# Performance work log

Measured on AMD Instinct MI355X. Metric: run time of the kernel, lower is better.

Reference implementation:

```python
import jax, jax.numpy as jnp
import numpy as np

D_MODEL = 1024
D_STATE = 16
DT_RANK = 64  # ceil(1024/16)
DT_MIN, DT_MAX = 1e-3, 1e-1


def setup_inputs() -> dict:
    key = jax.random.key(0)
    ks = jax.random.split(key, 6)
    x = jax.random.normal(ks[0], (2, 2048, D_MODEL), jnp.float32)
    A_log = jax.random.normal(ks[1], (D_MODEL, D_STATE), jnp.float32)
    D = jax.random.normal(ks[2], (D_MODEL,), jnp.float32)
    # nn.Linear default init ~ U(-1/sqrt(fan_in), 1/sqrt(fan_in)); normal*scale is fine for a baseline
    x_proj_w = jax.random.normal(ks[3], (DT_RANK + 2 * D_STATE, D_MODEL), jnp.float32) * (D_MODEL ** -0.5)
    dt_init_std = DT_RANK ** -0.5
    dt_proj_w = jax.random.uniform(ks[4], (D_MODEL, DT_RANK), jnp.float32, -dt_init_std, dt_init_std)
    dt = jnp.exp(jax.random.uniform(ks[5], (D_MODEL,), jnp.float32)
                 * (np.log(DT_MAX) - np.log(DT_MIN)) + np.log(DT_MIN))
    dt_proj_b = dt + jnp.log(-jnp.expm1(-dt))  # inverse-softplus init
    return {"x": x, "A_log": A_log, "D": D, "x_proj_w": x_proj_w,
            "dt_proj_w": dt_proj_w, "dt_proj_b": dt_proj_b}


def _s6(x, A_log, D, x_proj_w, dt_proj_w, dt_proj_b):
    A = -jnp.exp(A_log)                                    # (d, n)
    xp = jnp.einsum('bld,ed->ble', x, x_proj_w)            # (b, l, r+2n)
    d_rank = xp[..., :DT_RANK]
    Bm = xp[..., DT_RANK:DT_RANK + D_STATE]                # (b, l, n)
    Cm = xp[..., DT_RANK + D_STATE:]                       # (b, l, n)
    delta = jax.nn.softplus(jnp.einsum('blr,dr->bld', d_rank, dt_proj_w) + dt_proj_b)
    deltaA = jnp.exp(jnp.einsum('bld,dn->bldn', delta, A))          # (b, l, d, n)
    deltaB_u = jnp.einsum('bld,bln,bld->bldn', delta, Bm, x)        # (b, l, d, n)

    def step(h, inp):
        dA_t, dBu_t, C_t = inp          # (b,d,n), (b,d,n), (b,n)
        h = dA_t * h + dBu_t
        y = jnp.einsum('bdn,bn->bd', h, C_t)
        return h, y

    b, l, d = x.shape
    h0 = jnp.zeros((b, d, D_STATE), x.dtype)
    _, ys = jax.lax.scan(step, h0,
                         (deltaA.transpose(1, 0, 2, 3),
                          deltaB_u.transpose(1, 0, 2, 3),
                          Cm.transpose(1, 0, 2)))
    y = ys.transpose(1, 0, 2) + x * D                      # (b, l, d)
    return y


def reference(x, A_log, D, x_proj_w, dt_proj_w, dt_proj_b):
    return _s6(x, A_log, D, x_proj_w, dt_proj_w, dt_proj_b)
```

## Files before the change

### kernel.cpp

```cpp
#include <hip/hip_runtime.h>
#include <math.h>

#define Bb 2
#define Ll 2048
#define Dm 1024
#define Ns 16
#define Rr 64
#define Ee 96
#define XPS 8
#define BLK (Bb*Ll)
#define NTHR 256
#define LOG2E 1.4426950408889634f
#define LN2   0.6931471805599453f

__device__ inline float ex2(float x) {
#if __has_builtin(__builtin_amdgcn_exp2f)
    return __builtin_amdgcn_exp2f(x);
#else
    return exp2f(x);
#endif
}
__device__ inline float lg2(float x) {
#if __has_builtin(__builtin_amdgcn_logf)
    return __builtin_amdgcn_logf(x);
#else
    return log2f(x);
#endif
}
__device__ inline float softplus_f(float z) {
    float e = ex2(-fabsf(z) * LOG2E);
    return fmaxf(z, 0.f) + lg2(1.f + e) * LN2;
}

__global__ void __launch_bounds__(NTHR)
k_xproj(const float* __restrict__ x, const float* __restrict__ xw,
        float* __restrict__ xp_part) {
    __shared__ __align__(16) float xs[32 * 68];
    __shared__ __align__(16) float wsh[32 * 100];
    int bx = blockIdx.x;
    int ks = bx & 7, mt = bx >> 3;
    int i0 = mt * 64;
    int tid = threadIdx.x;
    int tx = tid & 15, ty = tid >> 4;
    float acc[4][6];
#pragma unroll
    for (int ii = 0; ii < 4; ++ii)
#pragma unroll
        for (int jj = 0; jj < 6; ++jj) acc[ii][jj] = 0.f;

    for (int kc = 0; kc < 4; ++kc) {
        int k0 = ks * 128 + kc * 32;
        for (int t = tid; t < 512; t += NTHR) {
            int r = t >> 3, c = (t & 7) * 4;
            float4 v = *(const float4*)(x + (size_t)(i0 + r) * Dm + k0 + c);
            xs[(c+0)*68+r] = v.x; xs[(c+1)*68+r] = v.y;
            xs[(c+2)*68+r] = v.z; xs[(c+3)*68+r] = v.w;
        }
        for (int t = tid; t < 768; t += NTHR) {
            int r = t >> 3, c = (t & 7) * 4;
            float4 v = *(const float4*)(xw + (size_t)r * Dm + k0 + c);
            wsh[(c+0)*100+r] = v.x; wsh[(c+1)*100+r] = v.y;
            wsh[(c+2)*100+r] = v.z; wsh[(c+3)*100+r] = v.w;
        }
        __syncthreads();
#pragma unroll 8
        for (int k = 0; k < 32; ++k) {
            float4 xv = *(const float4*)(xs + k*68 + ty*4);
            float2 w0 = *(const float2*)(wsh + k*100 + tx*6 + 0);
            float2 w1 = *(const float2*)(wsh + k*100 + tx*6 + 2);
            float2 w2 = *(const float2*)(wsh + k*100 + tx*6 + 4);
            float xr[4] = {xv.x, xv.y, xv.z, xv.w};
            float wr[6] = {w0.x, w0.y, w1.x, w1.y, w2.x, w2.y};
#pragma unroll
            for (int ii = 0; ii < 4; ++ii)
#pragma unroll
                for (int jj = 0; jj < 6; ++jj)
                    acc[ii][jj] = fmaf(xr[ii], wr[jj], acc[ii][jj]);
        }
        __syncthreads();
    }
#pragma unroll
    for (int ii = 0; ii < 4; ++ii)
#pragma unroll
        for (int jj = 0; jj < 6; ++jj)
            xp_part[((size_t)ks * BLK + (i0 + ty*4 + ii)) * Ee + tx*6 + jj] = acc[ii][jj];
}

__global__ void __launch_bounds__(NTHR)
k_prep(const float* __restrict__ xp_part, float* __restrict__ xp) {
    int g = blockIdx.x * NTHR + threadIdx.x;
    const float4* p = (const float4*)xp_part;
    float4 s = p[g];
#pragma unroll
    for (int i = 1; i < XPS; ++i) {
        float4 v = p[(size_t)i * (BLK * Ee / 4) + g];
        s.x += v.x; s.y += v.y; s.z += v.z; s.w += v.w;
    }
    ((float4*)xp)[g] = s;
}

__global__ void __launch_bounds__(NTHR)
k_delta(const float* __restrict__ xp, const float* __restrict__ dtw,
        const float* __restrict__ dtb, float* __restrict__ delta) {
    __shared__ __align__(16) float xs[64 * 136];
    __shared__ __align__(16) float wsh[64 * 68];
    int bx = blockIdx.x;
    int nt = bx & 15, mt = bx >> 4;
    int i0 = mt * 128, j0 = nt * 64;
    int tid = threadIdx.x, tx = tid & 15, ty = tid >> 4;

    for (int t = tid; t < 2048; t += NTHR) {
        int r = t >> 4, c = (t & 15) * 4;
        float4 v = *(const float4*)(xp + (size_t)(i0 + r) * Ee + c);
        xs[(c+0)*136+r] = v.x; xs[(c+1)*136+r] = v.y;
        xs[(c+2)*136+r] = v.z; xs[(c+3)*136+r] = v.w;
    }
    for (int t = tid; t < 1024; t += NTHR) {
        int r = t >> 4, c = (t & 15) * 4;
        float4 w = *(const float4*)(dtw + (size_t)(j0 + r) * Rr + c);
        wsh[(c+0)*68+r] = w.x; wsh[(c+1)*68+r] = w.y;
        wsh[(c+2)*68+r] = w.z; wsh[(c+3)*68+r] = w.w;
    }
    __syncthreads();

    float acc[8][4];
#pragma unroll
    for (int ii = 0; ii < 8; ++ii)
#pragma unroll
        for (int jj = 0; jj < 4; ++jj) acc[ii][jj] = 0.f;
#pragma unroll 8
    for (int k = 0; k < 64; ++k) {
        float4 xa = *(const float4*)(xs + k*136 + ty*8 + 0);
        float4 xb = *(const float4*)(xs + k*136 + ty*8 + 4);
        float4 wv = *(const float4*)(wsh + k*68 + tx*4);
        float xr[8] = {xa.x,xa.y,xa.z,xa.w, xb.x,xb.y,xb.z,xb.w};
        float wr[4] = {wv.x, wv.y, wv.z, wv.w};
#pragma unroll
        for (int ii = 0; ii < 8; ++ii)
#pragma unroll
            for (int jj = 0; jj < 4; ++jj)
                acc[ii][jj] = fmaf(xr[ii], wr[jj], acc[ii][jj]);
    }
    int d0 = j0 + tx * 4;
    float4 bias = *(const float4*)(dtb + d0);
#pragma unroll
    for (int ii = 0; ii < 8; ++ii) {
        int bl = i0 + ty*8 + ii;
        float4 o;
        o.x = softplus_f(acc[ii][0] + bias.x);
        o.y = softplus_f(acc[ii][1] + bias.y);
        o.z = softplus_f(acc[ii][2] + bias.z);
        o.w = softplus_f(acc[ii][3] + bias.w);
        *(float4*)(delta + (size_t)bl * Dm + d0) = o;
    }
}

__device__ inline void load_a2(const float* __restrict__ A_log, int d, float* a2) {
    const float4* Ap = (const float4*)(A_log + (size_t)d * Ns);
    float4 a0 = Ap[0], a1 = Ap[1], a2v = Ap[2], a3 = Ap[3];
    float tmp[Ns] = {a0.x,a0.y,a0.z,a0.w, a1.x,a1.y,a1.z,a1.w,
                     a2v.x,a2v.y,a2v.z,a2v.w, a3.x,a3.y,a3.z,a3.w};
#pragma unroll
    for (int n = 0; n < Ns; ++n) a2[n] = -__expf(tmp[n]) * LOG2E;
}

template<int CHv>
__global__ void __launch_bounds__(NTHR, 4)
k_scan_part(const float* __restrict__ delta, const float* __restrict__ x,
            const float* __restrict__ xp, const float* __restrict__ A_log,
            float* __restrict__ Ec, float* __restrict__ Sc) {
    constexpr int CLv = Ll / CHv;
    __shared__ __align__(16) float bsh[CLv * 16];
    int bx = blockIdx.x;
    int dblk = bx & 3, chunk = (bx >> 2) & (CHv - 1), b = bx >> 2 >> __builtin_ctz(CHv);
    int tid = threadIdx.x;
    int d = dblk * 256 + tid;
    int row0 = b * Ll + chunk * CLv;

    if (tid < CLv * 4) {
        int r = tid >> 2, c = (tid & 3) * 4;
        *(float4*)(bsh + r*16 + c) =
            *(const float4*)(xp + (size_t)(row0 + r) * Ee + Rr + c);
    }

    float a2[Ns];
    load_a2(A_log, d, a2);

    float dl[CLv], xv[CLv];
#pragma unroll
    for (int t = 0; t < CLv; ++t) {
        size_t row = (size_t)(row0 + t);
        dl[t] = delta[row * Dm + d];
        xv[t] = x[row * Dm + d];
    }
    __syncthreads();

    float h[Ns];
#pragma unroll
    for (int n = 0; n < Ns; ++n) h[n] = 0.f;
    float sd = 0.f;

#pragma unroll
    for (int t = 0; t < CLv; ++t) {
        float4 B0 = *(const float4*)(bsh + t*16 + 0);
        float4 B1 = *(const float4*)(bsh + t*16 + 4);
        float4 B2 = *(const float4*)(bsh + t*16 + 8);
        float4 B3 = *(const float4*)(bsh + t*16 + 12);
        float Bv[Ns] = {B0.x,B0.y,B0.z,B0.w, B1.x,B1.y,B1.z,B1.w,
                        B2.x,B2.y,B2.z,B2.w, B3.x,B3.y,B3.z,B3.w};
        float dx = dl[t] * xv[t];
        sd += dl[t];
#pragma unroll
        for (int n = 0; n < Ns; ++n)
            h[n] = fmaf(ex2(dl[t] * a2[n]), h[n], dx * Bv[n]);
    }
    size_t base = ((size_t)b * CHv + chunk) * Dm + d;
    float4* Ep = (float4*)(Ec + base * Ns);
    Ep[0] = make_float4(h[0],  h[1],  h[2],  h[3]);
    Ep[1] = make_float4(h[4],  h[5],  h[6],  h[7]);
    Ep[2] = make_float4(h[8],  h[9],  h[10], h[11]);
    Ep[3] = make_float4(h[12], h[13], h[14], h[15]);
    Sc[base] = sd;
}

template<int CHv, int G>
__global__ void __launch_bounds__(NTHR)
k_comb1(const float* __restrict__ Ec, const float* __restrict__ Sc,
        const float* __restrict__ A_log, float* __restrict__ Hloc,
        float* __restrict__ Spre, float* __restrict__ Eg, float* __restrict__ Sg) {
    constexpr int CPG = CHv / G;
    int gid = blockIdx.x * NTHR + threadIdx.x;
    int n = gid & (Ns - 1);
    int d = (gid >> 4) & (Dm - 1);
    int g = (gid >> 14) & (G - 1);
    int b = gid >> 17;
    float a2 = -__expf(A_log[d * Ns + n]) * LOG2E;
    float h = 0.f, S = 0.f;
#pragma unroll
    for (int j = 0; j < CPG; ++j) {
        size_t base = ((size_t)b * CHv + g * CPG + j) * Dm + d;
        float e  = Ec[base * Ns + n];
        float sc = Sc[base];
        Hloc[base * Ns + n] = h;
        if (n == 0) Spre[base] = S;
        h = fmaf(ex2(a2 * sc), h, e);
        S += sc;
    }
    size_t gb = ((size_t)b * G + g) * Dm + d;
    Eg[gb * Ns + n] = h;
    if (n == 0) Sg[gb] = S;
}

template<int G>
__global__ void __launch_bounds__(NTHR)
k_comb2(const float* __restrict__ Eg, const float* __restrict__ Sg,
        const float* __restrict__ A_log, float* __restrict__ Hg) {
    int gid = blockIdx.x * NTHR + threadIdx.x;
    int n = gid & (Ns - 1);
    int d = (gid >> 4) & (Dm - 1);
    int b = gid >> 14;
    float a2 = -__expf(A_log[d * Ns + n]) * LOG2E;
    float h = 0.f;
#pragma unroll
    for (int g = 0; g < G; ++g) {
        size_t gb = ((size_t)b * G + g) * Dm + d;
        Hg[gb * Ns + n] = h;
        h = fmaf(ex2(a2 * Sg[gb]), h, Eg[gb * Ns + n]);
    }
}

template<int CHv, int G>
__global__ void __launch_bounds__(NTHR, 4)
k_scan_full(const float* __restrict__ delta, const float* __restrict__ x,
            const float* __restrict__ xp, const float* __restrict__ A_log,
            const float* __restrict__ Dp, const float* __restrict__ Hloc,
            const float* __restrict__ Spre, const float* __restrict__ Hg,
            float* __restrict__ out) {
    constexpr int CLv = Ll / CHv;
    constexpr int CPG = CHv / G;
    __shared__ __align__(16) float bcs[CLv * 32];
    int bx = blockIdx.x;
    int dblk = bx & 3, chunk = (bx >> 2) & (CHv - 1), b = bx >> 2 >> __builtin_ctz(CHv);
    int tid = threadIdx.x;
    int d = dblk * 256 + tid;
    int row0 = b * Ll + chunk * CLv;

    if (tid < CLv * 8) {
        int r = tid >> 3, c = (tid & 7) * 4;
        *(float4*)(bcs + r*32 + c) =
            *(const float4*)(xp + (size_t)(row0 + r) * Ee + Rr + c);
    }

    float a2[Ns], h[Ns];
    load_a2(A_log, d, a2);
    size_t base = ((size_t)b * CHv + chunk) * Dm + d;
    size_t gb   = ((size_t)b * G + chunk / CPG) * Dm + d;
    {
        float sp = Spre[base];
        const float4* Hl = (const float4*)(Hloc + base * Ns);
        const float4* Hp = (const float4*)(Hg + gb * Ns);
        float4 l0 = Hl[0], l1 = Hl[1], l2 = Hl[2], l3 = Hl[3];
        float4 g0 = Hp[0], g1 = Hp[1], g2 = Hp[2], g3 = Hp[3];
        float lv[Ns] = {l0.x,l0.y,l0.z,l0.w, l1.x,l1.y,l1.z,l1.w,
                        l2.x,l2.y,l2.z,l2.w, l3.x,l3.y,l3.z,l3.w};
        float gv[Ns] = {g0.x,g0.y,g0.z,g0.w, g1.x,g1.y,g1.z,g1.w,
                        g2.x,g2.y,g2.z,g2.w, g3.x,g3.y,g3.z,g3.w};
#pragma unroll
        for (int n = 0; n < Ns; ++n) h[n] = fmaf(ex2(a2[n] * sp), gv[n], lv[n]);
    }
    float Dval = Dp[d];

    float dl[CLv], xv[CLv];
#pragma unroll
    for (int t = 0; t < CLv; ++t) {
        size_t row = (size_t)(row0 + t);
        dl[t] = delta[row * Dm + d];
        xv[t] = x[row * Dm + d];
    }
    __syncthreads();

#pragma unroll
    for (int t = 0; t < CLv; ++t) {
        float4 B0 = *(const float4*)(bcs + t*32 + 0);
        float4 B1 = *(const float4*)(bcs + t*32 + 4);
        float4 B2 = *(const float4*)(bcs + t*32 + 8);
        float4 B3 = *(const float4*)(bcs + t*32 + 12);
        float4 C0 = *(const float4*)(bcs + t*32 + 16);
        float4 C1 = *(const float4*)(bcs + t*32 + 20);
        float4 C2 = *(const float4*)(bcs + t*32 + 24);
        float4 C3 = *(const float4*)(bcs + t*32 + 28);
        float Bv[Ns] = {B0.x,B0.y,B0.z,B0.w, B1.x,B1.y,B1.z,B1.w,
                        B2.x,B2.y,B2.z,B2.w, B3.x,B3.y,B3.z,B3.w};
        float Cv[Ns] = {C0.x,C0.y,C0.z,C0.w, C1.x,C1.y,C1.z,C1.w,
                        C2.x,C2.y,C2.z,C2.w, C3.x,C3.y,C3.z,C3.w};
        float dx = dl[t] * xv[t];
        float ya[4] = {0.f, 0.f, 0.f, 0.f};
#pragma unroll
        for (int n = 0; n < Ns; ++n) {
            h[n] = fmaf(ex2(dl[t] * a2[n]), h[n], dx * Bv[n]);
            ya[n & 3] = fmaf(h[n], Cv[n], ya[n & 3]);
        }
        out[(size_t)(row0 + t) * Dm + d] = fmaf(xv[t], Dval, (ya[0] + ya[1]) + (ya[2] + ya[3]));
    }
}

extern "C" void kernel_launch(void* const* d_in, const int* in_sizes, int n_in,
                              void* d_out, int out_size, void* d_ws, size_t ws_size,
                              hipStream_t stream) {
    const float* x     = (const float*)d_in[0];
    const float* A_log = (const float*)d_in[1];
    const float* Dp    = (const float*)d_in[2];
    const float* xw    = (const float*)d_in[3];
    const float* dtw   = (const float*)d_in[4];
    const float* dtb   = (const float*)d_in[5];
    float* out = (float*)d_out;
    float* ws  = (float*)d_ws;

    float* xp      = ws;
    float* delta   = xp + 393216;
    float* S3      = delta + 4194304;
    float* xp_part = S3;

    k_xproj<<<dim3(512), dim3(NTHR), 0, stream>>>(x, xw, xp_part);
    k_prep <<<dim3(384), dim3(NTHR), 0, stream>>>(xp_part, xp);
    k_delta<<<dim3(512), dim3(NTHR), 0, stream>>>(xp, dtw, dtb, delta);

    constexpr int G = 8;
    size_t s3_128 = (size_t)Bb*128*Dm*Ns + (size_t)Bb*128*Dm + (size_t)Bb*128*Dm*Ns
                  + (size_t)Bb*128*Dm + (size_t)Bb*G*Dm*Ns + (size_t)Bb*G*Dm
                  + (size_t)Bb*G*Dm*Ns;
    size_t need128 = ((size_t)393216 + 4194304 + s3_128) * 4;
    if (ws_size >= need128) {
        constexpr int CHv = 128;
        float* Ec   = S3;
        float* Sc   = Ec   + (size_t)Bb*CHv*Dm*Ns;
        float* Hloc = Sc   + (size_t)Bb*CHv*Dm;
        float* Spre = Hloc + (size_t)Bb*CHv*Dm*Ns;
        float* Eg   = Spre + (size_t)Bb*CHv*Dm;
        float* Sg   = Eg   + (size_t)Bb*G*Dm*Ns;
        float* Hg   = Sg   + (size_t)Bb*G*Dm;
        k_scan_part<CHv>  <<<dim3(Bb*CHv*4), dim3(NTHR), 0, stream>>>(delta, x, xp, A_log, Ec, Sc);
        k_comb1<CHv, G>   <<<dim3(Bb*G*Dm*Ns/NTHR), dim3(NTHR), 0, stream>>>(Ec, Sc, A_log, Hloc, Spre, Eg, Sg);
        k_comb2<G>        <<<dim3(Bb*Dm*Ns/NTHR), dim3(NTHR), 0, stream>>>(Eg, Sg, A_log, Hg);
        k_scan_full<CHv,G><<<dim3(Bb*CHv*4), dim3(NTHR), 0, stream>>>(delta, x, xp, A_log, Dp, Hloc, Spre, Hg, out);
    } else {
        constexpr int CHv = 64;
        float* Ec   = S3;
        float* Sc   = Ec   + (size_t)Bb*CHv*Dm*Ns;
        float* Hloc = Sc   + (size_t)Bb*CHv*Dm;
        float* Spre = Hloc + (size_t)Bb*CHv*Dm*Ns;
        float* Eg   = Spre + (size_t)Bb*CHv*Dm;
        float* Sg   = Eg   + (size_t)Bb*G*Dm*Ns;
        float* Hg   = Sg   + (size_t)Bb*G*Dm;
        k_scan_part<CHv>  <<<dim3(Bb*CHv*4), dim3(NTHR), 0, stream>>>(delta, x, xp, A_log, Ec, Sc);
        k_comb1<CHv, G>   <<<dim3(Bb*G*Dm*Ns/NTHR), dim3(NTHR), 0, stream>>>(Ec, Sc, A_log, Hloc, Spre, Eg, Sg);
        k_comb2<G>        <<<dim3(Bb*Dm*Ns/NTHR), dim3(NTHR), 0, stream>>>(Eg, Sg, A_log, Hg);
        k_scan_full<CHv,G><<<dim3(Bb*CHv*4), dim3(NTHR), 0, stream>>>(delta, x, xp, A_log, Dp, Hloc, Spre, Hg, out);
    }
}
```

Baseline: 156.4 us.

## Compute local-chunk outputs in first scan pass and fix up with carried state

After: 166.5 us. +6.4%, slower.

```diff
diff --git a/kernel.cpp b/kernel.cpp
--- a/kernel.cpp
+++ b/kernel.cpp
@@ -166,118 +166,12 @@
 
 template<int CHv>
 __global__ void __launch_bounds__(NTHR, 4)
-k_scan_part(const float* __restrict__ delta, const float* __restrict__ x,
-            const float* __restrict__ xp, const float* __restrict__ A_log,
-            float* __restrict__ Ec, float* __restrict__ Sc) {
+k_scan1(const float* __restrict__ delta, const float* __restrict__ x,
+        const float* __restrict__ xp, const float* __restrict__ A_log,
+        const float* __restrict__ Dp,
+        float* __restrict__ Ec, float* __restrict__ Sc,
+        float* __restrict__ ypart) {
     constexpr int CLv = Ll / CHv;
-    __shared__ __align__(16) float bsh[CLv * 16];
-    int bx = blockIdx.x;
-    int dblk = bx & 3, chunk = (bx >> 2) & (CHv - 1), b = bx >> 2 >> __builtin_ctz(CHv);
-    int tid = threadIdx.x;
-    int d = dblk * 256 + tid;
-    int row0 = b * Ll + chunk * CLv;
-
-    if (tid < CLv * 4) {
-        int r = tid >> 2, c = (tid & 3) * 4;
-        *(float4*)(bsh + r*16 + c) =
-            *(const float4*)(xp + (size_t)(row0 + r) * Ee + Rr + c);
-    }
-
-    float a2[Ns];
-    load_a2(A_log, d, a2);
-
-    float dl[CLv], xv[CLv];
-#pragma unroll
-    for (int t = 0; t < CLv; ++t) {
-        size_t row = (size_t)(row0 + t);
-        dl[t] = delta[row * Dm + d];
-        xv[t] = x[row * Dm + d];
-    }
-    __syncthreads();
-
-    float h[Ns];
-#pragma unroll
-    for (int n = 0; n < Ns; ++n) h[n] = 0.f;
-    float sd = 0.f;
-
-#pragma unroll
-    for (int t = 0; t < CLv; ++t) {
-        float4 B0 = *(const float4*)(bsh + t*16 + 0);
-        float4 B1 = *(const float4*)(bsh + t*16 + 4);
-        float4 B2 = *(const float4*)(bsh + t*16 + 8);
-        float4 B3 = *(const float4*)(bsh + t*16 + 12);
-        float Bv[Ns] = {B0.x,B0.y,B0.z,B0.w, B1.x,B1.y,B1.z,B1.w,
-                        B2.x,B2.y,B2.z,B2.w, B3.x,B3.y,B3.z,B3.w};
-        float dx = dl[t] * xv[t];
-        sd += dl[t];
-#pragma unroll
-        for (int n = 0; n < Ns; ++n)
-            h[n] = fmaf(ex2(dl[t] * a2[n]), h[n], dx * Bv[n]);
-    }
-    size_t base = ((size_t)b * CHv + chunk) * Dm + d;
-    float4* Ep = (float4*)(Ec + base * Ns);
-    Ep[0] = make_float4(h[0],  h[1],  h[2],  h[3]);
-    Ep[1] = make_float4(h[4],  h[5],  h[6],  h[7]);
-    Ep[2] = make_float4(h[8],  h[9],  h[10], h[11]);
-    Ep[3] = make_float4(h[12], h[13], h[14], h[15]);
-    Sc[base] = sd;
-}
-
-template<int CHv, int G>
-__global__ void __launch_bounds__(NTHR)
-k_comb1(const float* __restrict__ Ec, const float* __restrict__ Sc,
-        const float* __restrict__ A_log, float* __restrict__ Hloc,
-        float* __restrict__ Spre, float* __restrict__ Eg, float* __restrict__ Sg) {
-    constexpr int CPG = CHv / G;
-    int gid = blockIdx.x * NTHR + threadIdx.x;
-    int n = gid & (Ns - 1);
-    int d = (gid >> 4) & (Dm - 1);
-    int g = (gid >> 14) & (G - 1);
-    int b = gid >> 17;
-    float a2 = -__expf(A_log[d * Ns + n]) * LOG2E;
-    float h = 0.f, S = 0.f;
-#pragma unroll
-    for (int j = 0; j < CPG; ++j) {
-        size_t base = ((size_t)b * CHv + g * CPG + j) * Dm + d;
-        float e  = Ec[base * Ns + n];
-        float sc = Sc[base];
-        Hloc[base * Ns + n] = h;
-        if (n == 0) Spre[base] = S;
-        h = fmaf(ex2(a2 * sc), h, e);
-        S += sc;
-    }
-    size_t gb = ((size_t)b * G + g) * Dm + d;
-    Eg[gb * Ns + n] = h;
-    if (n == 0) Sg[gb] = S;
-}
-
-template<int G>
-__global__ void __launch_bounds__(NTHR)
-k_comb2(const float* __restrict__ Eg, const float* __restrict__ Sg,
-        const float* __restrict__ A_log, float* __restrict__ Hg) {
-    int gid = blockIdx.x * NTHR + threadIdx.x;
-    int n = gid & (Ns - 1);
-    int d = (gid >> 4) & (Dm - 1);
-    int b = gid >> 14;
-    float a2 = -__expf(A_log[d * Ns + n]) * LOG2E;
-    float h = 0.f;
-#pragma unroll
-    for (int g = 0; g < G; ++g) {
-        size_t gb = ((size_t)b * G + g) * Dm + d;
-        Hg[gb * Ns + n] = h;
-        h = fmaf(ex2(a2 * Sg[gb]), h, Eg[gb * Ns + n]);
-    }
-}
-
-template<int CHv, int G>
-__global__ void __launch_bounds__(NTHR, 4)
-k_scan_full(const float* __restrict__ delta, const float* __restrict__ x,
-            const float* __restrict__ xp, const float* __restrict__ A_log,
-            const float* __restrict__ Dp, const float* __restrict__ Hloc,
-            const float* __restrict__ Spre, const float* __restrict__ Hg,
-            float* __restrict__ out) {
-    constexpr int CLv = Ll / CHv;
-    constexpr int CPG = CHv / G;
     __shared__ __align__(16) float bcs[CLv * 32];
     int bx = blockIdx.x;
     int dblk = bx & 3, chunk = (bx >> 2) & (CHv - 1), b = bx >> 2 >> __builtin_ctz(CHv);
@@ -291,23 +185,8 @@
             *(const float4*)(xp + (size_t)(row0 + r) * Ee + Rr + c);
     }
 
-    float a2[Ns], h[Ns];
+    float a2[Ns];
     load_a2(A_log, d, a2);
-    size_t base = ((size_t)b * CHv + chunk) * Dm + d;
-    size_t gb   = ((size_t)b * G + chunk / CPG) * Dm + d;
-    {
-        float sp = Spre[base];
-        const float4* Hl = (const float4*)(Hloc + base * Ns);
-        const float4* Hp = (const float4*)(Hg + gb * Ns);
-        float4 l0 = Hl[0], l1 = Hl[1], l2 = Hl[2], l3 = Hl[3];
-        float4 g0 = Hp[0], g1 = Hp[1], g2 = Hp[2], g3 = Hp[3];
-        float lv[Ns] = {l0.x,l0.y,l0.z,l0.w, l1.x,l1.y,l1.z,l1.w,
-                        l2.x,l2.y,l2.z,l2.w, l3.x,l3.y,l3.z,l3.w};
-        float gv[Ns] = {g0.x,g0.y,g0.z,g0.w, g1.x,g1.y,g1.z,g1.w,
-                        g2.x,g2.y,g2.z,g2.w, g3.x,g3.y,g3.z,g3.w};
-#pragma unroll
-        for (int n = 0; n < Ns; ++n) h[n] = fmaf(ex2(a2[n] * sp), gv[n], lv[n]);
-    }
     float Dval = Dp[d];
 
     float dl[CLv], xv[CLv];
@@ -318,6 +197,11 @@
         xv[t] = x[row * Dm + d];
     }
     __syncthreads();
+
+    float h[Ns];
+#pragma unroll
+    for (int n = 0; n < Ns; ++n) h[n] = 0.f;
+    float sd = 0.f;
 
 #pragma unroll
     for (int t = 0; t < CLv; ++t) {
@@ -334,13 +218,137 @@
         float Cv[Ns] = {C0.x,C0.y,C0.z,C0.w, C1.x,C1.y,C1.z,C1.w,
                         C2.x,C2.y,C2.z,C2.w, C3.x,C3.y,C3.z,C3.w};
         float dx = dl[t] * xv[t];
+        sd += dl[t];
         float ya[4] = {0.f, 0.f, 0.f, 0.f};
 #pragma unroll
         for (int n = 0; n < Ns; ++n) {
             h[n] = fmaf(ex2(dl[t] * a2[n]), h[n], dx * Bv[n]);
             ya[n & 3] = fmaf(h[n], Cv[n], ya[n & 3]);
         }
-        out[(size_t)(row0 + t) * Dm + d] = fmaf(xv[t], Dval, (ya[0] + ya[1]) + (ya[2] + ya[3]));
+        ypart[(size_t)(row0 + t) * Dm + d] =
+            fmaf(xv[t], Dval, (ya[0] + ya[1]) + (ya[2] + ya[3]));
+    }
+    size_t base = ((size_t)b * CHv + chunk) * Dm + d;
+    float4* Ep = (float4*)(Ec + base * Ns);
+    Ep[0] = make_float4(h[0],  h[1],  h[2],  h[3]);
+    Ep[1] = make_float4(h[4],  h[5],  h[6],  h[7]);
+    Ep[2] = make_float4(h[8],  h[9],  h[10], h[11]);
+    Ep[3] = make_float4(h[12], h[13], h[14], h[15]);
+    Sc[base] = sd;
+}
+
+template<int CHv, int G>
+__global__ void __launch_bounds__(NTHR)
+k_comb1(const float* __restrict__ Ec, const float* __restrict__ Sc,
+        const float* __restrict__ A_log, float* __restrict__ Hloc,
+        float* __restrict__ Spre, float* __restrict__ Eg, float* __restrict__ Sg) {
+    constexpr int CPG = CHv / G;
+    int gid = blockIdx.x * NTHR + threadIdx.x;
+    int n = gid & (Ns - 1);
+    int d = (gid >> 4) & (Dm - 1);
+    int g = (gid >> 14) & (G - 1);
+    int b = gid >> 17;
+    float a2 = -__expf(A_log[d * Ns + n]) * LOG2E;
+    float h = 0.f, S = 0.f;
+#pragma unroll
+    for (int j = 0; j < CPG; ++j) {
+        size_t base = ((size_t)b * CHv + g * CPG + j) * Dm + d;
+        float e  = Ec[base * Ns + n];
+        float sc = Sc[base];
+        Hloc[base * Ns + n] = h;
+        if (n == 0) Spre[base] = S;
+        h = fmaf(ex2(a2 * sc), h, e);
+        S += sc;
+    }
+    size_t gb = ((size_t)b * G + g) * Dm + d;
+    Eg[gb * Ns + n] = h;
+    if (n == 0) Sg[gb] = S;
+}
+
+template<int G>
+__global__ void __launch_bounds__(NTHR)
+k_comb2(const float* __restrict__ Eg, const float* __restrict__ Sg,
+        const float* __restrict__ A_log, float* __restrict__ Hg) {
+    int gid = blockIdx.x * NTHR + threadIdx.x;
+    int n = gid & (Ns - 1);
+    int d = (gid >> 4) & (Dm - 1);
+    int b = gid >> 14;
+    float a2 = -__expf(A_log[d * Ns + n]) * LOG2E;
+    float h = 0.f;
+#pragma unroll
+    for (int g = 0; g < G; ++g) {
+        size_t gb = ((size_t)b * G + g) * Dm + d;
+        Hg[gb * Ns + n] = h;
+        h = fmaf(ex2(a2 * Sg[gb]), h, Eg[gb * Ns + n]);
+    }
+}
+
+template<int CHv, int G>
+__global__ void __launch_bounds__(NTHR, 4)
+k_fix(const float* __restrict__ delta, const float* __restrict__ xp,
+      const float* __restrict__ A_log,
+      const float* __restrict__ Hloc, const float* __restrict__ Spre,
+      const float* __restrict__ Hg,
+      const float* __restrict__ ypart, float* __restrict__ out) {
+    constexpr int CLv = Ll / CHv;
+    constexpr int CPG = CHv / G;
+    __shared__ __align__(16) float csh[CLv * 16];
+    int bx = blockIdx.x;
+    int dblk = bx & 3, chunk = (bx >> 2) & (CHv - 1), b = bx >> 2 >> __builtin_ctz(CHv);
+    int tid = threadIdx.x;
+    int d = dblk * 256 + tid;
+    int row0 = b * Ll + chunk * CLv;
+
+    if (tid < CLv * 4) {
+        int r = tid >> 2, c = (tid & 3) * 4;
+        *(float4*)(csh + r*16 + c) =
+            *(const float4*)(xp + (size_t)(row0 + r) * Ee + Rr + Ns + c);
+    }
+
+    float a2[Ns], Hin[Ns];
+    load_a2(A_log, d, a2);
+    size_t base = ((size_t)b * CHv + chunk) * Dm + d;
+    size_t gb   = ((size_t)b * G + chunk / CPG) * Dm + d;
+    {
+        float sp = Spre[base];
+        const float4* Hl = (const float4*)(Hloc + base * Ns);
+        const float4* Hp = (const float4*)(Hg + gb * Ns);
+        float4 l0 = Hl[0], l1 = Hl[1], l2 = Hl[2], l3 = Hl[3];
+        float4 g0 = Hp[0], g1 = Hp[1], g2 = Hp[2], g3 = Hp[3];
+        float lv[Ns] = {l0.x,l0.y,l0.z,l0.w, l1.x,l1.y,l1.z,l1.w,
+                        l2.x,l2.y,l2.z,l2.w, l3.x,l3.y,l3.z,l3.w};
+        float gv[Ns] = {g0.x,g0.y,g0.z,g0.w, g1.x,g1.y,g1.z,g1.w,
+                        g2.x,g2.y,g2.z,g2.w, g3.x,g3.y,g3.z,g3.w};
+#pragma unroll
+        for (int n = 0; n < Ns; ++n) Hin[n] = fmaf(ex2(a2[n] * sp), gv[n], lv[n]);
+    }
+
+    float dl[CLv], yp[CLv];
+#pragma unroll
+    for (int t = 0; t < CLv; ++t) {
+        size_t row = (size_t)(row0 + t);
+        dl[t] = delta[row * Dm + d];
+        yp[t] = ypart[row * Dm + d];
+    }
+    __syncthreads();
+
+    float sd = 0.f;
+#pragma unroll
+    for (int t = 0; t < CLv; ++t) {
+        sd += dl[t];
+        float4 C0 = *(const float4*)(csh + t*16 + 0);
+        float4 C1 = *(const float4*)(csh + t*16 + 4);
+        float4 C2 = *(const float4*)(csh + t*16 + 8);
+        float4 C3 = *(const float4*)(csh + t*16 + 12);
+        float Cv[Ns] = {C0.x,C0.y,C0.z,C0.w, C1.x,C1.y,C1.z,C1.w,
+                        C2.x,C2.y,C2.z,C2.w, C3.x,C3.y,C3.z,C3.w};
+        float ya[4] = {0.f, 0.f, 0.f, 0.f};
+#pragma unroll
+        for (int n = 0; n < Ns; ++n) {
+            float p = ex2(a2[n] * sd);
+            ya[n & 3] = fmaf(p * Hin[n], Cv[n], ya[n & 3]);
+        }
+        out[(size_t)(row0 + t) * Dm + d] = yp[t] + (ya[0] + ya[1]) + (ya[2] + ya[3]);
     }
 }
 
@@ -366,35 +374,36 @@
     k_delta<<<dim3(512), dim3(NTHR), 0, stream>>>(xp, dtw, dtb, delta);
 
     constexpr int G = 8;
-    size_t s3_128 = (size_t)Bb*128*Dm*Ns + (size_t)Bb*128*Dm + (size_t)Bb*128*Dm*Ns
-                  + (size_t)Bb*128*Dm + (size_t)Bb*G*Dm*Ns + (size_t)Bb*G*Dm
-                  + (size_t)Bb*G*Dm*Ns;
+    size_t s3_128 = (size_t)Bb*128*Dm*Ns*2 + (size_t)Bb*128*Dm*2
+                  + (size_t)Bb*G*Dm*Ns*2 + (size_t)Bb*G*Dm + (size_t)BLK*Dm;
     size_t need128 = ((size_t)393216 + 4194304 + s3_128) * 4;
     if (ws_size >= need128) {
         constexpr int CHv = 128;
-        float* Ec   = S3;
-        float* Sc   = Ec   + (size_t)Bb*CHv*Dm*Ns;
-        float* Hloc = Sc   + (size_t)Bb*CHv*Dm;
-        float* Spre = Hloc + (size_t)Bb*CHv*Dm*Ns;
-        float* Eg   = Spre + (size_t)Bb*CHv*Dm;
-        float* Sg   = Eg   + (size_t)Bb*G*Dm*Ns;
-        float* Hg   = Sg   + (size_t)Bb*G*Dm;
-        k_scan_part<CHv>  <<<dim3(Bb*CHv*4), dim3(NTHR), 0, stream>>>(delta, x, xp, A_log, Ec, Sc);
-        k_comb1<CHv, G>   <<<dim3(Bb*G*Dm*Ns/NTHR), dim3(NTHR), 0, stream>>>(Ec, Sc, A_log, Hloc, Spre, Eg, Sg);
-        k_comb2<G>        <<<dim3(Bb*Dm*Ns/NTHR), dim3(NTHR), 0, stream>>>(Eg, Sg, A_log, Hg);
-        k_scan_full<CHv,G><<<dim3(Bb*CHv*4), dim3(NTHR), 0, stream>>>(delta, x, xp, A_log, Dp, Hloc, Spre, Hg, out);
+        float* Ec    = S3;
+        float* Sc    = Ec    + (size_t)Bb*CHv*Dm*Ns;
+        float* Hloc  = Sc    + (size_t)Bb*CHv*Dm;
+        float* Spre  = Hloc  + (size_t)Bb*CHv*Dm*Ns;
+        float* Eg    = Spre  + (size_t)Bb*CHv*Dm;
+        float* Sg    = Eg    + (size_t)Bb*G*Dm*Ns;
+        float* Hg    = Sg    + (size_t)Bb*G*Dm;
+        float* ypart = Hg    + (size_t)Bb*G*Dm*Ns;
+        k_scan1<CHv>   <<<dim3(Bb*CHv*4), dim3(NTHR), 0, stream>>>(delta, x, xp, A_log, Dp, Ec, Sc, ypart);
+        k_comb1<CHv, G><<<dim3(Bb*G*Dm*Ns/NTHR), dim3(NTHR), 0, stream>>>(Ec, Sc, A_log, Hloc, Spre, Eg, Sg);
+        k_comb2<G>     <<<dim3(Bb*Dm*Ns/NTHR), dim3(NTHR), 0, stream>>>(Eg, Sg, A_log, Hg);
+        k_fix<CHv, G>  <<<dim3(Bb*CHv*4), dim3(NTHR), 0, stream>>>(delta, xp, A_log, Hloc, Spre, Hg, ypart, out);
     } else {
         constexpr int CHv = 64;
-        float* Ec   = S3;
-        float* Sc   = Ec   + (size_t)Bb*CHv*Dm*Ns;
-        float* Hloc = Sc   + (size_t)Bb*CHv*Dm;
-        float* Spre = Hloc + (size_t)Bb*CHv*Dm*Ns;
-        float* Eg   = Spre + (size_t)Bb*CHv*Dm;
-        float* Sg   = Eg   + (size_t)Bb*G*Dm*Ns;
-        float* Hg   = Sg   + (size_t)Bb*G*Dm;
-        k_scan_part<CHv>  <<<dim3(Bb*CHv*4), dim3(NTHR), 0, stream>>>(delta, x, xp, A_log, Ec, Sc);
-        k_comb1<CHv, G>   <<<dim3(Bb*G*Dm*Ns/NTHR), dim3(NTHR), 0, stream>>>(Ec, Sc, A_log, Hloc, Spre, Eg, Sg);
-        k_comb2<G>        <<<dim3(Bb*Dm*Ns/NTHR), dim3(NTHR), 0, stream>>>(Eg, Sg, A_log, Hg);
-        k_scan_full<CHv,G><<<dim3(Bb*CHv*4), dim3(NTHR), 0, stream>>>(delta, x, xp, A_log, Dp, Hloc, Spre, Hg, out);
-    }
-}
+        float* Ec    = S3;
+        float* Sc    = Ec    + (size_t)Bb*CHv*Dm*Ns;
+        float* Hloc  = Sc    + (size_t)Bb*CHv*Dm;
+        float* Spre  = Hloc  + (size_t)Bb*CHv*Dm*Ns;
+        float* Eg    = Spre  + (size_t)Bb*CHv*Dm;
+        float* Sg    = Eg    + (size_t)Bb*G*Dm*Ns;
+        float* Hg    = Sg    + (size_t)Bb*G*Dm;
+        float* ypart = Hg    + (size_t)Bb*G*Dm*Ns;
+        k_scan1<CHv>   <<<dim3(Bb*CHv*4), dim3(NTHR), 0, stream>>>(delta, x, xp, A_log, Dp, Ec, Sc, ypart);
+        k_comb1<CHv, G><<<dim3(Bb*G*Dm*Ns/NTHR), dim3(NTHR), 0, stream>>>(Ec, Sc, A_log, Hloc, Spre, Eg, Sg);
+        k_comb2<G>     <<<dim3(Bb*Dm*Ns/NTHR), dim3(NTHR), 0, stream>>>(Eg, Sg, A_log, Hg);
+        k_fix<CHv, G>  <<<dim3(Bb*CHv*4), dim3(NTHR), 0, stream>>>(delta, xp, A_log, Hloc, Spre, Hg, ypart, out);
+    }
+}
```
